# Optimization experiments

Hardware: AMD Instinct MI355X
Metric: run time of the kernel (lower is better)

The kernel has to match this reference:

```python
import jax, jax.numpy as jnp
import numpy as np

N, D = 8192, 128
TEMPERATURE = 128.0


def setup_inputs() -> dict:
    key = jax.random.key(0)
    kx, ka = jax.random.split(key)
    x = jax.random.normal(kx, (N, D), dtype=jnp.float32)
    a = jax.random.normal(ka, (N, D), dtype=jnp.float32)
    return {"x": x, "a": a}


def reference(x, a):
    """uLSIF loss, 2D branch, exp_parameterization='inner_product', reduction='mean'.

    L_i = -2 * sim[i,i] + mean_{j != i} sim[i,j]^2,  sim = exp(x @ a.T / T)
    """
    n = x.shape[0]
    sim = jnp.exp(jnp.matmul(x, a.T) / TEMPERATURE)  # [N, N]
    sim_pos = jnp.diagonal(sim)                      # [N]
    # off-diagonal squared mean without a boolean-mask gather:
    # sum_j sim[i,j]^2 - sim[i,i]^2, divided by (N-1)
    row_sq_sum = jnp.sum(sim * sim, axis=1)          # [N]
    sim_neg_square = (row_sq_sum - sim_pos * sim_pos) / (n - 1)
    lora_loss = -2.0 * sim_pos + sim_neg_square      # [N]
    return jnp.mean(lora_loss)
```

## Files before the change

### kernel.cpp

```cpp
#include <hip/hip_runtime.h>


#define NN 8192
#define DD 128
#define NT 8

typedef __attribute__((ext_vector_type(4))) float f32x4;
typedef __attribute__((ext_vector_type(8))) _Float16 f16x8;

__device__ __forceinline__ void gload_lds16(const void* g, void* l) {
    __builtin_amdgcn_global_load_lds(
        (const __attribute__((address_space(1))) void*)g,
        (__attribute__((address_space(3))) void*)l, 16, 0, 0);
}

__device__ __forceinline__ void block_sync() {
    asm volatile("" ::: "memory");
    __builtin_amdgcn_s_barrier();
    asm volatile("" ::: "memory");
}

__global__ void conv_diag_kernel(const float4* __restrict__ x, const float4* __restrict__ a,
                                 ushort4* __restrict__ xb, ushort4* __restrict__ ab,
                                 double* __restrict__ s1p, double* __restrict__ s3p) {
    const float C2 = (float)(2.0 / (128.0 * 0.69314718055994530942));
    int t = threadIdx.x;
    int i = blockIdx.x * 256 + t;
    float4 xv = x[i];
    float4 av = a[i];
    ushort4 xu, au;
    xu.x = __builtin_bit_cast(unsigned short, (_Float16)xv.x);
    xu.y = __builtin_bit_cast(unsigned short, (_Float16)xv.y);
    xu.z = __builtin_bit_cast(unsigned short, (_Float16)xv.z);
    xu.w = __builtin_bit_cast(unsigned short, (_Float16)xv.w);
    au.x = __builtin_bit_cast(unsigned short, (_Float16)(av.x * C2));
    au.y = __builtin_bit_cast(unsigned short, (_Float16)(av.y * C2));
    au.z = __builtin_bit_cast(unsigned short, (_Float16)(av.z * C2));
    au.w = __builtin_bit_cast(unsigned short, (_Float16)(av.w * C2));
    xb[i] = xu;
    ab[i] = au;

    float d = xv.x * av.x + xv.y * av.y + xv.z * av.z + xv.w * av.w;
#pragma unroll
    for (int off = 16; off > 0; off >>= 1) d += __shfl_down(d, off, 32);

    __shared__ double rr[8];
    if ((t & 31) == 0) rr[t >> 5] = exp((double)d * (1.0 / 128.0));
    __syncthreads();
    if (t == 0) {
        double s1 = 0.0, s3 = 0.0;
#pragma unroll
        for (int k = 0; k < 8; ++k) { s1 += rr[k]; s3 += rr[k] * rr[k]; }
        s1p[blockIdx.x] = s1;
        s3p[blockIdx.x] = s3;
    }
}

__global__ __launch_bounds__(512, 2) void gemm_exp_sum(const ushort* __restrict__ xb,
                                                       const ushort* __restrict__ ab,
                                                       double* __restrict__ s2p) {
    __shared__ char smem[131072];
    char* As    = smem;
    char* Bbuf  = smem + 65536;

    const int tid  = threadIdx.x;
    const int lane = tid & 63;
    const int wid  = tid >> 6;
    const int bm    = blockIdx.x >> 3;
    const int chunk = blockIdx.x & 7;

    const char* gA  = (const char*)(xb + (size_t)bm * 256 * DD);
    const char* gB0 = (const char*)(ab + (size_t)chunk * (NT * 128) * DD);

    const int t16 = tid * 16;

    {
        char* ldsA = As + wid * 1024;
#pragma unroll
        for (int i = 0; i < 8; ++i) {
            int off = i * 8192 + t16;
            int row = off >> 8;
            int src = (row << 8) | ((off & 255) ^ ((row & 7) << 4));
            gload_lds16(gA + src, ldsA + i * 8192);
        }
        char* ldsB = Bbuf + wid * 1024;
#pragma unroll
        for (int i = 0; i < 4; ++i) {
            int off = i * 8192 + t16;
            int row = off >> 8;
            int src = (row << 8) | ((off & 255) ^ ((row & 7) << 4));
            gload_lds16(gB0 + src, ldsB + i * 8192);
        }
    }
    asm volatile("s_waitcnt vmcnt(4)" ::: "memory");
    block_sync();

    const int wr = (wid >> 1) * 64;
    const int wc = (wid & 1) * 64;
    const int rl = lane & 15;
    const int kq = (lane >> 4) * 16;
    f16x8 af[4][4];
#pragma unroll
    for (int mi = 0; mi < 4; ++mi)
#pragma unroll
        for (int ks = 0; ks < 4; ++ks) {
            int r  = wr + mi * 16 + rl;
            int cb = ks * 64 + kq;
            af[mi][ks] = *(const f16x8*)(As + r * 256 + (cb ^ ((r & 7) << 4)));
        }

    float ls0 = 0.f, ls1 = 0.f, ls2 = 0.f, ls3 = 0.f;

#pragma unroll
    for (int t = 0; t < NT; ++t) {
        const char* Bs = Bbuf + (t & 1) * 32768;

        if (t + 1 < NT) {
            const char* gB  = gB0 + (size_t)(t + 1) * 128 * DD * 2;
            char* ldsB = Bbuf + ((t + 1) & 1) * 32768 + wid * 1024;
#pragma unroll
            for (int i = 0; i < 4; ++i) {
                int off = i * 8192 + t16;
                int row = off >> 8;
                int src = (row << 8) | ((off & 255) ^ ((row & 7) << 4));
                gload_lds16(gB + src, ldsB + i * 8192);
            }
            asm volatile("s_waitcnt vmcnt(4)" ::: "memory");
        } else {
            asm volatile("s_waitcnt vmcnt(0)" ::: "memory");
        }
        block_sync();

        f32x4 acc[4][4];
#pragma unroll
        for (int mi = 0; mi < 4; ++mi)
#pragma unroll
            for (int ni = 0; ni < 4; ++ni)
                acc[mi][ni] = f32x4{0.f, 0.f, 0.f, 0.f};

#pragma unroll
        for (int ks = 0; ks < 4; ++ks) {
            f16x8 bfr[4];
#pragma unroll
            for (int ni = 0; ni < 4; ++ni) {
                int r  = wc + ni * 16 + rl;
                int cb = ks * 64 + kq;
                bfr[ni] = *(const f16x8*)(Bs + r * 256 + (cb ^ ((r & 7) << 4)));
            }
#pragma unroll
            for (int mi = 0; mi < 4; ++mi)
#pragma unroll
                for (int ni = 0; ni < 4; ++ni)
                    acc[mi][ni] = __builtin_amdgcn_mfma_f32_16x16x32_f16(
                        af[mi][ks], bfr[ni], acc[mi][ni], 0, 0, 0);
        }

#pragma unroll
        for (int mi = 0; mi < 4; ++mi)
#pragma unroll
            for (int ni = 0; ni < 4; ++ni) {
                ls0 += __builtin_amdgcn_exp2f(acc[mi][ni][0]);
                ls1 += __builtin_amdgcn_exp2f(acc[mi][ni][1]);
                ls2 += __builtin_amdgcn_exp2f(acc[mi][ni][2]);
                ls3 += __builtin_amdgcn_exp2f(acc[mi][ni][3]);
            }

        block_sync();
    }

    float lsum = (ls0 + ls1) + (ls2 + ls3);
#pragma unroll
    for (int off = 32; off > 0; off >>= 1) lsum += __shfl_down(lsum, off);

    double* wred = (double*)smem;
    if (lane == 0) wred[wid] = (double)lsum;
    __syncthreads();
    if (tid == 0) {
        double s = 0.0;
#pragma unroll
        for (int k = 0; k < 8; ++k) s += wred[k];
        s2p[blockIdx.x] = s;
    }
}

__global__ void finalize_kernel(const double* __restrict__ s1p, const double* __restrict__ s3p,
                                const double* __restrict__ s2p, float* __restrict__ out) {
    int t = threadIdx.x;
    double v1 = s1p[t];
    double v3 = s3p[t];
    double v2 = (t < 256) ? s2p[t] : 0.0;
#pragma unroll
    for (int off = 32; off > 0; off >>= 1) {
        v1 += __shfl_down(v1, off);
        v3 += __shfl_down(v3, off);
        v2 += __shfl_down(v2, off);
    }
    __shared__ double r1[16], r2[16], r3[16];
    int wid = t >> 6, lane = t & 63;
    if (lane == 0) { r1[wid] = v1; r2[wid] = v2; r3[wid] = v3; }
    __syncthreads();
    if (t == 0) {
        double S1 = 0.0, S2 = 0.0, S3 = 0.0;
#pragma unroll
        for (int k = 0; k < 16; ++k) { S1 += r1[k]; S2 += r2[k]; S3 += r3[k]; }
        double res = (-2.0 * S1 + (S2 - S3) / (double)(NN - 1)) / (double)NN;
        out[0] = (float)res;
    }
}

extern "C" void kernel_launch(void* const* d_in, const int* in_sizes, int n_in,
                              void* d_out, int out_size, void* d_ws, size_t ws_size,
                              hipStream_t stream) {
    const float* x = (const float*)d_in[0];
    const float* a = (const float*)d_in[1];
    float* out = (float*)d_out;
    char* ws = (char*)d_ws;

    double* s1p = (double*)ws;
    double* s3p = (double*)(ws + 8192);
    double* s2p = (double*)(ws + 16384);
    ushort* xb  = (ushort*)(ws + 32768);
    ushort* ab  = (ushort*)(ws + 32768 + (size_t)NN * DD * 2);

    conv_diag_kernel<<<1024, 256, 0, stream>>>((const float4*)x, (const float4*)a,
                                               (ushort4*)xb, (ushort4*)ab, s1p, s3p);
    gemm_exp_sum<<<256, 512, 0, stream>>>(xb, ab, s2p);
    finalize_kernel<<<1, 1024, 0, stream>>>(s1p, s3p, s2p, out);
}
```

Measured before the change: 83.19 us.

## Pre-swizzle operands into MFMA fragment layout and load directly to registers

The conversion kernel now writes x and scaled a as f16 in a fragment-major layout that matches the 16x16x32 MFMA operand order. The GEMM kernel then drops LDS staging and barriers and loads fragments straight from global memory into registers, using a three-slot rotating prefetch of B fragments. The diagonal computation is split into its own kernel. This removes LDS traffic and block syncs, but it adds an extra launch, leans on L2 for B reuse across waves, and exposes global load latency that the shallow prefetch may not fully hide.

```diff
diff --git a/kernel.cpp b/kernel.cpp
--- a/kernel.cpp
+++ b/kernel.cpp
@@ -3,47 +3,44 @@
 
 #define NN 8192
 #define DD 128
-#define NT 8
 
 typedef __attribute__((ext_vector_type(4))) float f32x4;
 typedef __attribute__((ext_vector_type(8))) _Float16 f16x8;
 
-__device__ __forceinline__ void gload_lds16(const void* g, void* l) {
-    __builtin_amdgcn_global_load_lds(
-        (const __attribute__((address_space(1))) void*)g,
-        (__attribute__((address_space(3))) void*)l, 16, 0, 0);
+__global__ void convert_kernel(const float4* __restrict__ x, const float4* __restrict__ a,
+                               f16x8* __restrict__ xf, f16x8* __restrict__ af) {
+    const float C2 = (float)(2.0 / (128.0 * 0.69314718055994530942));
+    int j  = blockIdx.x * 256 + threadIdx.x;
+    int m  = j >> 17;
+    int jj = j & 131071;
+    int f  = jj >> 6;
+    int l  = jj & 63;
+    int rg = f >> 2, ks = f & 3;
+    int row = rg * 16 + (l & 15);
+    int kf  = ks * 32 + (l >> 4) * 8;
+    int base = row * 32 + (kf >> 2);
+    const float4* in = m ? a : x;
+    float4 v0 = in[base];
+    float4 v1 = in[base + 1];
+    float s = m ? C2 : 1.0f;
+    f16x8 o;
+    o[0] = (_Float16)(v0.x * s); o[1] = (_Float16)(v0.y * s);
+    o[2] = (_Float16)(v0.z * s); o[3] = (_Float16)(v0.w * s);
+    o[4] = (_Float16)(v1.x * s); o[5] = (_Float16)(v1.y * s);
+    o[6] = (_Float16)(v1.z * s); o[7] = (_Float16)(v1.w * s);
+    (m ? af : xf)[(size_t)f * 64 + l] = o;
 }
 
-__device__ __forceinline__ void block_sync() {
-    asm volatile("" ::: "memory");
-    __builtin_amdgcn_s_barrier();
-    asm volatile("" ::: "memory");
-}
-
-__global__ void conv_diag_kernel(const float4* __restrict__ x, const float4* __restrict__ a,
-                                 ushort4* __restrict__ xb, ushort4* __restrict__ ab,
-                                 double* __restrict__ s1p, double* __restrict__ s3p) {
-    const float C2 = (float)(2.0 / (128.0 * 0.69314718055994530942));
+__global__ void diag_kernel(const float4* __restrict__ x, const float4* __restrict__ a,
+                            double* __restrict__ s1p, double* __restrict__ s3p) {
     int t = threadIdx.x;
-    int i = blockIdx.x * 256 + t;
-    float4 xv = x[i];
-    float4 av = a[i];
-    ushort4 xu, au;
-    xu.x = __builtin_bit_cast(unsigned short, (_Float16)xv.x);
-    xu.y = __builtin_bit_cast(unsigned short, (_Float16)xv.y);
-    xu.z = __builtin_bit_cast(unsigned short, (_Float16)xv.z);
-    xu.w = __builtin_bit_cast(unsigned short, (_Float16)xv.w);
-    au.x = __builtin_bit_cast(unsigned short, (_Float16)(av.x * C2));
-    au.y = __builtin_bit_cast(unsigned short, (_Float16)(av.y * C2));
-    au.z = __builtin_bit_cast(unsigned short, (_Float16)(av.z * C2));
-    au.w = __builtin_bit_cast(unsigned short, (_Float16)(av.w * C2));
-    xb[i] = xu;
-    ab[i] = au;
-
+    int row = blockIdx.x * 8 + (t >> 5);
+    int c = t & 31;
+    float4 xv = x[row * 32 + c];
+    float4 av = a[row * 32 + c];
     float d = xv.x * av.x + xv.y * av.y + xv.z * av.z + xv.w * av.w;
 #pragma unroll
     for (int off = 16; off > 0; off >>= 1) d += __shfl_down(d, off, 32);
-
     __shared__ double rr[8];
     if ((t & 31) == 0) rr[t >> 5] = exp((double)d * (1.0 / 128.0));
     __syncthreads();
@@ -56,123 +53,75 @@
     }
 }
 
-__global__ __launch_bounds__(512, 2) void gemm_exp_sum(const ushort* __restrict__ xb,
-                                                       const ushort* __restrict__ ab,
+__global__ __launch_bounds__(512, 2) void gemm_exp_sum(const f16x8* __restrict__ xf,
+                                                       const f16x8* __restrict__ af,
                                                        double* __restrict__ s2p) {
-    __shared__ char smem[131072];
-    char* As    = smem;
-    char* Bbuf  = smem + 65536;
-
     const int tid  = threadIdx.x;
     const int lane = tid & 63;
     const int wid  = tid >> 6;
     const int bm    = blockIdx.x >> 3;
     const int chunk = blockIdx.x & 7;
+    const int wm = wid >> 1;
+    const int wn = wid & 1;
 
-    const char* gA  = (const char*)(xb + (size_t)bm * 256 * DD);
-    const char* gB0 = (const char*)(ab + (size_t)chunk * (NT * 128) * DD);
-
-    const int t16 = tid * 16;
-
-    {
-        char* ldsA = As + wid * 1024;
-#pragma unroll
-        for (int i = 0; i < 8; ++i) {
-            int off = i * 8192 + t16;
-            int row = off >> 8;
-            int src = (row << 8) | ((off & 255) ^ ((row & 7) << 4));
-            gload_lds16(gA + src, ldsA + i * 8192);
-        }
-        char* ldsB = Bbuf + wid * 1024;
-#pragma unroll
-        for (int i = 0; i < 4; ++i) {
-            int off = i * 8192 + t16;
-            int row = off >> 8;
-            int src = (row << 8) | ((off & 255) ^ ((row & 7) << 4));
-            gload_lds16(gB0 + src, ldsB + i * 8192);
-        }
-    }
-    asm volatile("s_waitcnt vmcnt(4)" ::: "memory");
-    block_sync();
-
-    const int wr = (wid >> 1) * 64;
-    const int wc = (wid & 1) * 64;
-    const int rl = lane & 15;
-    const int kq = (lane >> 4) * 16;
-    f16x8 af[4][4];
+    const int fA0 = (bm * 16 + wm * 4) * 4;
+    f16x8 afr[4][4];
 #pragma unroll
     for (int mi = 0; mi < 4; ++mi)
 #pragma unroll
-        for (int ks = 0; ks < 4; ++ks) {
-            int r  = wr + mi * 16 + rl;
-            int cb = ks * 64 + kq;
-            af[mi][ks] = *(const f16x8*)(As + r * 256 + (cb ^ ((r & 7) << 4)));
-        }
+        for (int ks = 0; ks < 4; ++ks)
+            afr[mi][ks] = xf[(size_t)(fA0 + mi * 4 + ks) * 64 + lane];
 
+    const int fB0 = (chunk * 64 + wn * 4) * 4;
+    f16x8 bfr[3][4];
+#pragma unroll
+    for (int kk = 0; kk < 3; ++kk)
+#pragma unroll
+        for (int ni = 0; ni < 4; ++ni)
+            bfr[kk][ni] = af[(size_t)(fB0 + ni * 4 + kk) * 64 + lane];
+
+    f32x4 acc[4][4];
+#pragma unroll
+    for (int mi = 0; mi < 4; ++mi)
+#pragma unroll
+        for (int ni = 0; ni < 4; ++ni) acc[mi][ni] = f32x4{0.f, 0.f, 0.f, 0.f};
     float ls0 = 0.f, ls1 = 0.f, ls2 = 0.f, ls3 = 0.f;
 
 #pragma unroll
-    for (int t = 0; t < NT; ++t) {
-        const char* Bs = Bbuf + (t & 1) * 32768;
-
-        if (t + 1 < NT) {
-            const char* gB  = gB0 + (size_t)(t + 1) * 128 * DD * 2;
-            char* ldsB = Bbuf + ((t + 1) & 1) * 32768 + wid * 1024;
-#pragma unroll
-            for (int i = 0; i < 4; ++i) {
-                int off = i * 8192 + t16;
-                int row = off >> 8;
-                int src = (row << 8) | ((off & 255) ^ ((row & 7) << 4));
-                gload_lds16(gB + src, ldsB + i * 8192);
-            }
-            asm volatile("s_waitcnt vmcnt(4)" ::: "memory");
-        } else {
-            asm volatile("s_waitcnt vmcnt(0)" ::: "memory");
-        }
-        block_sync();
-
-        f32x4 acc[4][4];
+    for (int kk = 0; kk < 32; ++kk) {
+        const int ks = kk & 3;
+        const int sl = kk % 3;
 #pragma unroll
         for (int mi = 0; mi < 4; ++mi)
 #pragma unroll
             for (int ni = 0; ni < 4; ++ni)
-                acc[mi][ni] = f32x4{0.f, 0.f, 0.f, 0.f};
-
+                acc[mi][ni] = __builtin_amdgcn_mfma_f32_16x16x32_f16(
+                    afr[mi][ks], bfr[sl][ni], acc[mi][ni], 0, 0, 0);
+        if (kk + 3 < 32) {
+            const int kn = kk + 3, tn = kn >> 2, ksn = kn & 3;
 #pragma unroll
-        for (int ks = 0; ks < 4; ++ks) {
-            f16x8 bfr[4];
-#pragma unroll
-            for (int ni = 0; ni < 4; ++ni) {
-                int r  = wc + ni * 16 + rl;
-                int cb = ks * 64 + kq;
-                bfr[ni] = *(const f16x8*)(Bs + r * 256 + (cb ^ ((r & 7) << 4)));
-            }
+            for (int ni = 0; ni < 4; ++ni)
+                bfr[sl][ni] = af[(size_t)(fB0 + tn * 32 + ni * 4 + ksn) * 64 + lane];
+        }
+        if (ks == 3) {
 #pragma unroll
             for (int mi = 0; mi < 4; ++mi)
 #pragma unroll
-                for (int ni = 0; ni < 4; ++ni)
-                    acc[mi][ni] = __builtin_amdgcn_mfma_f32_16x16x32_f16(
-                        af[mi][ks], bfr[ni], acc[mi][ni], 0, 0, 0);
+                for (int ni = 0; ni < 4; ++ni) {
+                    ls0 += __builtin_amdgcn_exp2f(acc[mi][ni][0]);
+                    ls1 += __builtin_amdgcn_exp2f(acc[mi][ni][1]);
+                    ls2 += __builtin_amdgcn_exp2f(acc[mi][ni][2]);
+                    ls3 += __builtin_amdgcn_exp2f(acc[mi][ni][3]);
+                    acc[mi][ni] = f32x4{0.f, 0.f, 0.f, 0.f};
+                }
         }
-
-#pragma unroll
-        for (int mi = 0; mi < 4; ++mi)
-#pragma unroll
-            for (int ni = 0; ni < 4; ++ni) {
-                ls0 += __builtin_amdgcn_exp2f(acc[mi][ni][0]);
-                ls1 += __builtin_amdgcn_exp2f(acc[mi][ni][1]);
-                ls2 += __builtin_amdgcn_exp2f(acc[mi][ni][2]);
-                ls3 += __builtin_amdgcn_exp2f(acc[mi][ni][3]);
-            }
-
-        block_sync();
     }
 
     float lsum = (ls0 + ls1) + (ls2 + ls3);
 #pragma unroll
     for (int off = 32; off > 0; off >>= 1) lsum += __shfl_down(lsum, off);
 
-    double* wred = (double*)smem;
+    __shared__ double wred[8];
     if (lane == 0) wred[wid] = (double)lsum;
     __syncthreads();
     if (tid == 0) {
@@ -219,11 +168,11 @@
     double* s1p = (double*)ws;
     double* s3p = (double*)(ws + 8192);
     double* s2p = (double*)(ws + 16384);
-    ushort* xb  = (ushort*)(ws + 32768);
-    ushort* ab  = (ushort*)(ws + 32768 + (size_t)NN * DD * 2);
+    f16x8*  xf  = (f16x8*)(ws + 32768);
+    f16x8*  af  = (f16x8*)(ws + 32768 + (size_t)NN * DD * 2);
 
-    conv_diag_kernel<<<1024, 256, 0, stream>>>((const float4*)x, (const float4*)a,
-                                               (ushort4*)xb, (ushort4*)ab, s1p, s3p);
-    gemm_exp_sum<<<256, 512, 0, stream>>>(xb, ab, s2p);
+    convert_kernel<<<1024, 256, 0, stream>>>((const float4*)x, (const float4*)a, xf, af);
+    diag_kernel<<<1024, 256, 0, stream>>>((const float4*)x, (const float4*)a, s1p, s3p);
+    gemm_exp_sum<<<256, 512, 0, stream>>>(xf, af, s2p);
     finalize_kernel<<<1, 1024, 0, stream>>>(s1p, s3p, s2p, out);
 }
```

Result: slower. 85.30 us (+2.5%).
